# Optimization experiments

Measured on AMD Instinct MI355X. Metric: run time of the kernel, lower is better.

Reference implementation:

```python
import jax, jax.numpy as jnp
import numpy as np

B, T, D_IN, H, K, C = 8, 2048, 512, 384, 8192, 8
N_BLOCKS = 6
EPS = 1e-5


def conv1d(x, w, b, pad, groups=1):
    # x: [B, Cin, T], w: [Cout, Cin//groups, k]
    y = jax.lax.conv_general_dilated(
        x, w, window_strides=(1,), padding=[(pad, pad)],
        dimension_numbers=("NCH", "OIH", "NCH"), feature_group_count=groups)
    return y + b[None, :, None]


def layernorm(x, g, b):
    # normalize over last axis
    m = jnp.mean(x, axis=-1, keepdims=True)
    v = jnp.mean(jnp.square(x - m), axis=-1, keepdims=True)
    return (x - m) * jax.lax.rsqrt(v + EPS) * g + b


def setup_inputs() -> dict:
    key = jax.random.key(0)
    ks = iter(jax.random.split(key, 32))
    s = 0.02
    inp = {
        "x": jax.random.normal(next(ks), (B, T, D_IN), dtype=jnp.float32),
        "enc_w": jax.random.normal(next(ks), (H, D_IN, 7)) * s,
        "enc_b": jnp.zeros((H,)),
        "enc_ln_g": jnp.ones((H,)),
        "enc_ln_b": jnp.zeros((H,)),
        "blk_dw_w": jax.random.normal(next(ks), (N_BLOCKS, H, 1, 7)) * s,
        "blk_dw_b": jnp.zeros((N_BLOCKS, H)),
        "blk_ln_g": jnp.ones((N_BLOCKS, H)),
        "blk_ln_b": jnp.zeros((N_BLOCKS, H)),
        "blk_w1": jax.random.normal(next(ks), (N_BLOCKS, 4 * H, H)) * s,
        "blk_b1": jnp.zeros((N_BLOCKS, 4 * H)),
        "blk_w2": jax.random.normal(next(ks), (N_BLOCKS, H, 4 * H)) * s,
        "blk_b2": jnp.zeros((N_BLOCKS, H)),
        "out_w": jax.random.normal(next(ks), (C, H, 1)) * s,
        "out_b": jnp.zeros((C,)),
        "embeddings": jax.random.normal(next(ks), (K, C)),
    }
    return inp


def encode(x, enc_w, enc_b, enc_ln_g, enc_ln_b, blk_dw_w, blk_dw_b,
           blk_ln_g, blk_ln_b, blk_w1, blk_b1, blk_w2, blk_b2, out_w, out_b):
    h = x.transpose(0, 2, 1)                       # [B, D_IN, T]
    h = conv1d(h, enc_w, enc_b, pad=3)             # [B, H, T]
    h = layernorm(h.transpose(0, 2, 1), enc_ln_g, enc_ln_b).transpose(0, 2, 1)
    for i in range(N_BLOCKS):
        res = h
        h = conv1d(h, blk_dw_w[i], blk_dw_b[i], pad=3, groups=H)  # depthwise
        ht = h.transpose(0, 2, 1)                  # [B, T, H]
        ht = layernorm(ht, blk_ln_g[i], blk_ln_b[i])
        ht = jnp.einsum("bth,fh->btf", ht, blk_w1[i]) + blk_b1[i]
        ht = jax.nn.gelu(ht, approximate=False)    # torch GELU is exact erf
        ht = jnp.einsum("btf,hf->bth", ht, blk_w2[i]) + blk_b2[i]
        h = ht.transpose(0, 2, 1) + res
    z = conv1d(h, out_w, out_b, pad=0)             # [B, C, T]
    return z.transpose(0, 2, 1)                    # [B, T, C]


def reference(x, enc_w, enc_b, enc_ln_g, enc_ln_b, blk_dw_w, blk_dw_b,
              blk_ln_g, blk_ln_b, blk_w1, blk_b1, blk_w2, blk_b2,
              out_w, out_b, embeddings):
    z = encode(x, enc_w, enc_b, enc_ln_g, enc_ln_b, blk_dw_w, blk_dw_b,
               blk_ln_g, blk_ln_b, blk_w1, blk_b1, blk_w2, blk_b2, out_w, out_b)
    flat = z.reshape(-1, C)                        # [B*T, C]
    # squared euclidean distances: same argmin as torch.cdist
    d2 = (jnp.sum(flat * flat, axis=1, keepdims=True)
          - 2.0 * flat @ embeddings.T
          + jnp.sum(embeddings * embeddings, axis=1))  # [B*T, K]
    indices = jnp.argmin(d2, axis=1)               # [B*T], int
    return indices
```

## Files before the change

### kernel.cpp

```cpp
#include <hip/hip_runtime.h>
#include <math.h>

#define T_   2048
#define DIN  512
#define H_   384
#define H4_  1536
#define BT_  16384

typedef _Float16 half_t;
typedef _Float16 f16x8 __attribute__((ext_vector_type(8)));
typedef float f32x4 __attribute__((ext_vector_type(4)));

#define LO_SCALE 2048.0f
#define LO_INV   4.8828125e-4f

__device__ __forceinline__ void lds_barrier() {
    asm volatile("s_waitcnt lgkmcnt(0)\n\ts_barrier" ::: "memory");
}

__device__ __forceinline__ void split2(float v, half_t* hi, half_t* lo) {
    half_t h = (half_t)v;
    *hi = h;
    *lo = (half_t)((v - (float)h) * LO_SCALE);
}

__global__ void k_split(const float* __restrict__ in, half_t* __restrict__ hi,
                        half_t* __restrict__ lo, long n) {
    long i = (long)blockIdx.x * 256 + threadIdx.x;
    if (i >= n) return;
    split2(in[i], hi + i, lo + i);
}

__global__ void k_split_encw(const float* __restrict__ in, half_t* __restrict__ hi,
                             half_t* __restrict__ lo) {
    int idx = blockIdx.x * 256 + threadIdx.x;
    if (idx >= H_ * 3584) return;
    int n = idx / 3584;
    int r = idx % 3584;
    int tap = r >> 9, i = r & 511;
    split2(in[n * 3584 + i * 7 + tap], hi + idx, lo + idx);
}

__global__ void k_ln(const float* __restrict__ in, float* __restrict__ out,
                     const float* __restrict__ g, const float* __restrict__ b) {
    int row = blockIdx.x;
    int lane = threadIdx.x;
    const float* ir = in + (long)row * H_;
    float v[6];
    float s = 0.f;
#pragma unroll
    for (int j = 0; j < 6; ++j) { v[j] = ir[lane + (j << 6)]; s += v[j]; }
#pragma unroll
    for (int o = 32; o > 0; o >>= 1) s += __shfl_down(s, o, 64);
    s = __shfl(s, 0, 64);
    float mean = s * (1.f / 384.f);
    float q = 0.f;
#pragma unroll
    for (int j = 0; j < 6; ++j) { float d = v[j] - mean; q += d * d; }
#pragma unroll
    for (int o = 32; o > 0; o >>= 1) q += __shfl_down(q, o, 64);
    q = __shfl(q, 0, 64);
    float rstd = rsqrtf(q * (1.f / 384.f) + 1e-5f);
    float* orow = out + (long)row * H_;
#pragma unroll
    for (int j = 0; j < 6; ++j) {
        int c = lane + (j << 6);
        orow[c] = (v[j] - mean) * rstd * g[c] + b[c];
    }
}

__global__ __launch_bounds__(256) void k_dwconv_ln(
    const float* __restrict__ h, half_t* __restrict__ oh,
    half_t* __restrict__ ol,
    const float* __restrict__ w, const float* __restrict__ wb,
    const float* __restrict__ g, const float* __restrict__ gb) {
    int row = (blockIdx.x << 2) + (threadIdx.x >> 6);
    int b = row >> 11;
    int t = row & 2047;
    int lane = threadIdx.x & 63;
    const float* hb = h + ((long)b * T_) * H_;
    float vx[3], vy[3];
    float s = 0.f;
#pragma unroll
    for (int j = 0; j < 3; ++j) {
        int c = (lane << 1) + (j << 7);
        float ax = wb[c], ay = wb[c + 1];
        const float* wcx = w + c * 7;
        const float* wcy = wcx + 7;
#pragma unroll
        for (int k = 0; k < 7; ++k) {
            int tt = t + k - 3;
            if ((unsigned)tt < (unsigned)T_) {
                float2 hv = *(const float2*)&hb[(long)tt * H_ + c];
                ax = fmaf(hv.x, wcx[k], ax);
                ay = fmaf(hv.y, wcy[k], ay);
            }
        }
        vx[j] = ax; vy[j] = ay;
        s += ax + ay;
    }
#pragma unroll
    for (int o = 32; o > 0; o >>= 1) s += __shfl_down(s, o, 64);
    s = __shfl(s, 0, 64);
    float mean = s * (1.f / 384.f);
    float q = 0.f;
#pragma unroll
    for (int j = 0; j < 3; ++j) {
        float dx = vx[j] - mean, dy = vy[j] - mean;
        q += dx * dx + dy * dy;
    }
#pragma unroll
    for (int o = 32; o > 0; o >>= 1) q += __shfl_down(q, o, 64);
    q = __shfl(q, 0, 64);
    float rstd = rsqrtf(q * (1.f / 384.f) + 1e-5f);
    long ro = (long)row * H_;
#pragma unroll
    for (int j = 0; j < 3; ++j) {
        int c = (lane << 1) + (j << 7);
        float valx = (vx[j] - mean) * rstd * g[c] + gb[c];
        float valy = (vy[j] - mean) * rstd * g[c + 1] + gb[c + 1];
        split2(valx, oh + ro + c, ol + ro + c);
        split2(valy, oh + ro + c + 1, ol + ro + c + 1);
    }
}

#define DECLSET(S) float4 pAh##S, pAl##S, pBh0##S, pBl0##S, pBh1##S, pBl1##S

#define LOADREGS(S, k0_) do {                                               \
    int k0v = (k0_);                                                        \
    if (MODE == 0) {                                                        \
        int kk = k0v + ak;                                                  \
        int tap = kk >> 9, ii = kk & 511;                                   \
        int ta = tt0 + tap;                                                 \
        pAh##S = pAl##S = make_float4(0.f, 0.f, 0.f, 0.f);                  \
        if ((unsigned)ta < 2048u) {                                         \
            long o = ((long)bq * 2048 + ta) * 512 + ii;                     \
            pAh##S = *(const float4*)(Ah + o);                              \
            pAl##S = *(const float4*)(Al + o);                              \
        }                                                                   \
    } else {                                                                \
        pAh##S = *(const float4*)(Ah + aoff + k0v);                         \
        pAl##S = *(const float4*)(Al + aoff + k0v);                         \
    }                                                                       \
    pBh0##S = *(const float4*)(Bh + boff0 + k0v);                           \
    pBl0##S = *(const float4*)(Bl + boff0 + k0v);                           \
    pBh1##S = *(const float4*)(Bh + boff1 + k0v);                           \
    pBl1##S = *(const float4*)(Bl + boff1 + k0v);                           \
} while (0)

#define STOREBUF(S, buf) do {                                               \
    *(float4*)&smem[(buf) * 2048 + aw] = pAh##S;                            \
    *(float4*)&smem[4096 + (buf) * 2048 + aw] = pAl##S;                     \
    int b_ = 8192 + (buf) * 4096 + aw;                                      \
    *(float4*)&smem[b_] = pBh0##S;                                          \
    *(float4*)&smem[b_ + 2048] = pBh1##S;                                   \
    *(float4*)&smem[b_ + 8192] = pBl0##S;                                   \
    *(float4*)&smem[b_ + 8192 + 2048] = pBl1##S;                            \
} while (0)

template <int MODE, int NN>
__global__ __launch_bounds__(256, 3) void k_mgemm64(
    const half_t* __restrict__ Ah, const half_t* __restrict__ Al,
    const half_t* __restrict__ Bh, const half_t* __restrict__ Bl,
    const float* __restrict__ bias, const float* __restrict__ res,
    float* __restrict__ Cf, half_t* __restrict__ Ch, half_t* __restrict__ Cl,
    int N, int K) {
    __shared__ __align__(16) half_t smem[24576];
    const int tid = threadIdx.x;
    const int lane = tid & 63, wid = tid >> 6;
    const int wn = wid << 5;
    const int quad = lane >> 4, l16 = lane & 15;

    constexpr int NWG = 256 * NN;
    constexpr int CHUNK = NWG / 8;
    const int lin = blockIdx.x;
    const int tile = (lin & 7) * CHUNK + (lin >> 3);
    const int m0 = (tile / NN) << 6;
    const int n0 = (tile % NN) << 7;

    const int ar = tid >> 2;
    const int ak = (tid & 3) << 3;

    long aoff = 0;
    int tt0 = 0, bq = 0;
    if (MODE == 0) {
        bq = m0 >> 11;
        tt0 = (m0 & 2047) + ar - 3;
    } else {
        aoff = (long)(m0 + ar) * K + ak;
    }
    const long boff0 = (long)(n0 + ar) * K + ak;
    const long boff1 = boff0 + (long)64 * K;

    const int aw = ar * 32 + ((((tid & 3) ^ (ar >> 1)) & 3) << 3);

    DECLSET(0);
    DECLSET(1);

    f32x4 acc1[4][2] = {};
    f32x4 acc2[4][2] = {};
    const int sw = ((quad ^ (l16 >> 1)) & 3) << 3;

    auto compute = [&](int buf) {
        const int ab = buf * 2048 + l16 * 32 + sw;
        const int bb = 8192 + buf * 4096 + (wn + l16) * 32 + sw;
        f16x8 fah[4], fal[4], fgh[2], fgl[2];
#pragma unroll
        for (int f = 0; f < 4; ++f) {
            fah[f] = *(const f16x8*)&smem[ab + f * 512];
            fal[f] = *(const f16x8*)&smem[ab + 4096 + f * 512];
        }
#pragma unroll
        for (int g = 0; g < 2; ++g) {
            fgh[g] = *(const f16x8*)&smem[bb + g * 512];
            fgl[g] = *(const f16x8*)&smem[bb + 8192 + g * 512];
        }
#pragma unroll
        for (int f = 0; f < 4; ++f)
#pragma unroll
            for (int g = 0; g < 2; ++g)
                acc2[f][g] = __builtin_amdgcn_mfma_f32_16x16x32_f16(fah[f], fgl[g], acc2[f][g], 0, 0, 0);
#pragma unroll
        for (int f = 0; f < 4; ++f)
#pragma unroll
            for (int g = 0; g < 2; ++g)
                acc2[f][g] = __builtin_amdgcn_mfma_f32_16x16x32_f16(fal[f], fgh[g], acc2[f][g], 0, 0, 0);
#pragma unroll
        for (int f = 0; f < 4; ++f)
#pragma unroll
            for (int g = 0; g < 2; ++g)
                acc1[f][g] = __builtin_amdgcn_mfma_f32_16x16x32_f16(fah[f], fgh[g], acc1[f][g], 0, 0, 0);
    };

    const int nIter = K >> 5;
    LOADREGS(0, 0);
    LOADREGS(1, 32);
    STOREBUF(0, 0);
    if (nIter > 2) LOADREGS(0, 64);
    for (int it = 0; it < nIter; it += 2) {
        lds_barrier();
        compute(0);
        STOREBUF(1, 1);
        if (it + 3 < nIter) LOADREGS(1, (it + 3) << 5);
        lds_barrier();
        compute(1);
        if (it + 2 < nIter) {
            STOREBUF(0, 0);
            if (it + 4 < nIter) LOADREGS(0, (it + 4) << 5);
        }
    }

    float bv[2];
    bv[0] = bias[n0 + wn + l16];
    bv[1] = bias[n0 + wn + 16 + l16];

#pragma unroll
    for (int f = 0; f < 4; ++f)
#pragma unroll
        for (int g = 0; g < 2; ++g)
#pragma unroll
            for (int r = 0; r < 4; ++r) {
                long row = m0 + f * 16 + quad * 4 + r;
                int col = n0 + wn + g * 16 + l16;
                float v = acc1[f][g][r] + acc2[f][g][r] * LO_INV + bv[g];
                long o = row * N + col;
                if (MODE == 2) v += res[o];
                Cf[o] = v;
            }
}

#define LOADW8(k0_) do {                                                    \
    int k0v = (k0_);                                                        \
    qAh = *(const float4*)(Ah + aoff + k0v);                                \
    qAl = *(const float4*)(Al + aoff + k0v);                                \
    if (tid < 384) {                                                        \
        qBh = *(const float4*)(Bh + boff + k0v);                            \
        qBl = *(const float4*)(Bl + boff + k0v);                            \
    }                                                                       \
} while (0)

#define STOREW8(buf) do {                                                   \
    int a_ = (buf) * 14336 + sa;                                            \
    *(float4*)&smem[a_] = qAh;                                              \
    *(float4*)&smem[a_ + 4096] = qAl;                                       \
    if (tid < 384) {                                                        \
        int b_ = (buf) * 14336 + 8192 + sa;                                 \
        *(float4*)&smem[b_] = qBh;                                          \
        *(float4*)&smem[b_ + 3072] = qBl;                                   \
    }                                                                       \
} while (0)

template <int MODE, int NT>
__global__ __launch_bounds__(512, 4) void k_mgemm96w8(
    const half_t* __restrict__ Ah, const half_t* __restrict__ Al,
    const half_t* __restrict__ Bh, const half_t* __restrict__ Bl,
    const float* __restrict__ bias, const float* __restrict__ res,
    float* __restrict__ Cf, half_t* __restrict__ Ch, half_t* __restrict__ Cl,
    int N, int K) {
    __shared__ __align__(16) half_t smem[28672];
    const int tid = threadIdx.x;
    const int lane = tid & 63, wid = tid >> 6;
    const int wm = (wid >> 1) << 5;
    const int wn = (wid & 1) * 48;
    const int quad = lane >> 4, l16 = lane & 15;

    constexpr int NWG = 128 * NT;
    constexpr int CHUNK = NWG / 8;
    const int lin = blockIdx.x;
    const int tile = (lin & 7) * CHUNK + (lin >> 3);
    const int m0 = (tile / NT) << 7;
    const int n0 = (tile % NT) * 96;

    const int srow = tid >> 2;
    const int sg = tid & 3;
    const int sa = srow * 32 + (((sg ^ (tid >> 3)) & 3) << 3);

    const long aoff = (long)(m0 + srow) * K + (sg << 3);
    const long boff = (long)(n0 + srow) * K + (sg << 3);

    float4 qAh, qAl, qBh, qBl;

    f32x4 acc1[2][3] = {};
    f32x4 acc2[2][3] = {};
    const int sw = ((quad ^ (l16 >> 1)) & 3) << 3;

    auto compute = [&](int buf) {
        const int ab = buf * 14336 + (wm + l16) * 32 + sw;
        const int bb = buf * 14336 + 8192 + (wn + l16) * 32 + sw;
        f16x8 fah[2], fal[2], fgh[3], fgl[3];
#pragma unroll
        for (int f = 0; f < 2; ++f) {
            fah[f] = *(const f16x8*)&smem[ab + f * 512];
            fal[f] = *(const f16x8*)&smem[ab + 4096 + f * 512];
        }
#pragma unroll
        for (int g = 0; g < 3; ++g) {
            fgh[g] = *(const f16x8*)&smem[bb + g * 512];
            fgl[g] = *(const f16x8*)&smem[bb + 3072 + g * 512];
        }
#pragma unroll
        for (int f = 0; f < 2; ++f)
#pragma unroll
            for (int g = 0; g < 3; ++g)
                acc2[f][g] = __builtin_amdgcn_mfma_f32_16x16x32_f16(fah[f], fgl[g], acc2[f][g], 0, 0, 0);
#pragma unroll
        for (int f = 0; f < 2; ++f)
#pragma unroll
            for (int g = 0; g < 3; ++g)
                acc2[f][g] = __builtin_amdgcn_mfma_f32_16x16x32_f16(fal[f], fgh[g], acc2[f][g], 0, 0, 0);
#pragma unroll
        for (int f = 0; f < 2; ++f)
#pragma unroll
            for (int g = 0; g < 3; ++g)
                acc1[f][g] = __builtin_amdgcn_mfma_f32_16x16x32_f16(fah[f], fgh[g], acc1[f][g], 0, 0, 0);
    };

    const int nIter = K >> 5;
    LOADW8(0);
    STOREW8(0);
    int cur = 0;
    for (int it = 0; it < nIter; ++it) {
        if (it + 1 < nIter) LOADW8((it + 1) << 5);
        lds_barrier();
        compute(cur);
        if (it + 1 < nIter) STOREW8(cur ^ 1);
        cur ^= 1;
    }

    float bv[3];
#pragma unroll
    for (int g = 0; g < 3; ++g) bv[g] = bias[n0 + wn + g * 16 + l16];

    if (MODE == 1) {
        __syncthreads();
#pragma unroll
        for (int f = 0; f < 2; ++f)
#pragma unroll
            for (int g = 0; g < 3; ++g)
#pragma unroll
                for (int r = 0; r < 4; ++r) {
                    int rm = wm + f * 16 + quad * 4 + r;
                    int cn = wn + g * 16 + l16;
                    float v = acc1[f][g][r] + acc2[f][g][r] * LO_INV + bv[g];
                    v = 0.5f * v * (1.0f + erff(v * 0.70710678118654752f));
                    half_t hh = (half_t)v;
                    smem[rm * 104 + cn] = hh;
                    smem[13312 + rm * 104 + cn] = (half_t)((v - (float)hh) * LO_SCALE);
                }
        __syncthreads();
        int row = tid >> 2, c0 = (tid & 3) * 24;
        long go = (long)(m0 + row) * N + n0 + c0;
        int so = row * 104 + c0;
#pragma unroll
        for (int u = 0; u < 3; ++u) {
            *(float4*)(Ch + go + u * 8) = *(const float4*)&smem[so + u * 8];
            *(float4*)(Cl + go + u * 8) = *(const float4*)&smem[13312 + so + u * 8];
        }
    } else {
#pragma unroll
        for (int f = 0; f < 2; ++f)
#pragma unroll
            for (int g = 0; g < 3; ++g)
#pragma unroll
                for (int r = 0; r < 4; ++r) {
                    long row = m0 + wm + f * 16 + quad * 4 + r;
                    int col = n0 + wn + g * 16 + l16;
                    float v = acc1[f][g][r] + acc2[f][g][r] * LO_INV + bv[g];
                    long o = row * N + col;
                    v += res[o];
                    Cf[o] = v;
                }
    }
}

__global__ __launch_bounds__(256) void k_outconv_argmin(
    const float* __restrict__ h, const float* __restrict__ ow,
    const float* __restrict__ ob, const float* __restrict__ emb,
    int* __restrict__ outIdx) {
    __shared__ float hs[16][H_ + 1];
    __shared__ float zs[16][8];
    __shared__ float es[16 * 516];
    __shared__ float rb[16][16];
    __shared__ int ri[16][16];
    const int tid = threadIdx.x;
    const int row0 = blockIdx.x << 4;

    for (int i = tid; i < 16 * (H_ / 4); i += 256) {
        int r = i / 96;
        int c4 = (i % 96) << 2;
        float4 v = *(const float4*)&h[((long)(row0 + r)) * H_ + c4];
        hs[r][c4] = v.x; hs[r][c4 + 1] = v.y; hs[r][c4 + 2] = v.z; hs[r][c4 + 3] = v.w;
    }
    __syncthreads();

    if (tid < 128) {
        int r = tid & 15, c = tid >> 4;
        float acc = ob[c];
        const float* wc = ow + c * H_;
        for (int j = 0; j < H_; ++j) acc = fmaf(hs[r][j], wc[j], acc);
        zs[r][c] = acc;
    }
    __syncthreads();

    const int r = tid & 15;
    const int sl = tid >> 4;
    float z0 = zs[r][0], z1 = zs[r][1], z2 = zs[r][2], z3 = zs[r][3];
    float z4 = zs[r][4], z5 = zs[r][5], z6 = zs[r][6], z7 = zs[r][7];
    float best = 3.4e38f;
    int bi = 0;

    for (int ch = 0; ch < 8; ++ch) {
        __syncthreads();
        for (int i = tid; i < 2048; i += 256) {
            int e = i >> 1;
            int half = (i & 1) << 2;
            float4 src = *(const float4*)&emb[(((long)(ch << 10)) + e) * 8 + half];
            *(float4*)&es[(e >> 6) * 516 + ((e & 63) << 3) + half] = src;
        }
        __syncthreads();
        const float* ep = es + sl * 516;
        int gbase = (ch << 10) + (sl << 6);
#pragma unroll 4
        for (int j = 0; j < 64; ++j) {
            float4 e0 = *(const float4*)(ep + (j << 3));
            float4 e1 = *(const float4*)(ep + (j << 3) + 4);
            float t, d;
            t = e0.x - z0; d = t * t;
            t = e0.y - z1; d = fmaf(t, t, d);
            t = e0.z - z2; d = fmaf(t, t, d);
            t = e0.w - z3; d = fmaf(t, t, d);
            t = e1.x - z4; d = fmaf(t, t, d);
            t = e1.y - z5; d = fmaf(t, t, d);
            t = e1.z - z6; d = fmaf(t, t, d);
            t = e1.w - z7; d = fmaf(t, t, d);
            if (d < best) { best = d; bi = gbase + j; }
        }
    }
    rb[r][sl] = best;
    ri[r][sl] = bi;
    __syncthreads();
    if (sl == 0) {
        float bb = rb[r][0];
        int bbi = ri[r][0];
#pragma unroll
        for (int s2 = 1; s2 < 16; ++s2) {
            float v = rb[r][s2];
            int i2 = ri[r][s2];
            if (v < bb || (v == bb && i2 < bbi)) { bb = v; bbi = i2; }
        }
        outIdx[row0 + r] = bbi;
    }
}

extern "C" void kernel_launch(void* const* d_in, const int* in_sizes, int n_in,
                              void* d_out, int out_size, void* d_ws, size_t ws_size,
                              hipStream_t stream) {
    const float* x        = (const float*)d_in[0];
    const float* enc_w    = (const float*)d_in[1];
    const float* enc_b    = (const float*)d_in[2];
    const float* enc_ln_g = (const float*)d_in[3];
    const float* enc_ln_b = (const float*)d_in[4];
    const float* blk_dw_w = (const float*)d_in[5];
    const float* blk_dw_b = (const float*)d_in[6];
    const float* blk_ln_g = (const float*)d_in[7];
    const float* blk_ln_b = (const float*)d_in[8];
    const float* blk_w1   = (const float*)d_in[9];
    const float* blk_b1   = (const float*)d_in[10];
    const float* blk_w2   = (const float*)d_in[11];
    const float* blk_b2   = (const float*)d_in[12];
    const float* out_w    = (const float*)d_in[13];
    const float* out_b    = (const float*)d_in[14];
    const float* emb      = (const float*)d_in[15];
    int* out = (int*)d_out;

    char* base = (char*)d_ws;
    float*  h    = (float*)base;
    half_t* tmph = (half_t*)(base + 25165824);
    half_t* tmpl = (half_t*)(base + 37748736);
    half_t* ht4h = (half_t*)(base + 50331648);
    half_t* ht4l = (half_t*)(base + 100663296);
    half_t* ench = (half_t*)(base + 150994944);
    half_t* encl = (half_t*)(base + 153747456);
    half_t* w1h  = (half_t*)(base + 156499968);
    half_t* w1l  = (half_t*)(base + 163577856);
    half_t* w2h  = (half_t*)(base + 170655744);
    half_t* w2l  = (half_t*)(base + 177733632);
    half_t* xh = ht4h;
    half_t* xl = (half_t*)(base + 50331648 + 16777216);

    k_split<<<(8388608 + 255) / 256, 256, 0, stream>>>(x, xh, xl, 8388608L);
    k_split<<<(3538944 + 255) / 256, 256, 0, stream>>>(blk_w1, w1h, w1l, 3538944L);
    k_split<<<(3538944 + 255) / 256, 256, 0, stream>>>(blk_w2, w2h, w2l, 3538944L);
    k_split_encw<<<(H_ * 3584 + 255) / 256, 256, 0, stream>>>(enc_w, ench, encl);

    k_mgemm64<0, 3><<<768, 256, 0, stream>>>(xh, xl, ench, encl, enc_b,
                                             nullptr, h, nullptr, nullptr,
                                             H_, 3584);
    k_ln<<<BT_, 64, 0, stream>>>(h, h, enc_ln_g, enc_ln_b);

    for (int i = 0; i < 6; ++i) {
        k_dwconv_ln<<<BT_ / 4, 256, 0, stream>>>(h, tmph, tmpl, blk_dw_w + i * H_ * 7,
                                                 blk_dw_b + i * H_, blk_ln_g + i * H_,
                                                 blk_ln_b + i * H_);
        k_mgemm96w8<1, 16><<<2048, 512, 0, stream>>>(
            tmph, tmpl, w1h + (long)i * 589824, w1l + (long)i * 589824,
            blk_b1 + i * H4_, nullptr, nullptr, ht4h, ht4l, H4_, H_);
        k_mgemm96w8<2, 4><<<512, 512, 0, stream>>>(
            ht4h, ht4l, w2h + (long)i * 589824, w2l + (long)i * 589824,
            blk_b2 + i * H_, h, h, nullptr, nullptr, H_, H4_);
    }

    k_outconv_argmin<<<BT_ / 16, 256, 0, stream>>>(h, out_w, out_b, emb, out);
}
```

Measured before the change: 1.690 ms.

## Use 128x128 GEMM tiles with direct global-to-LDS DMA loads

Replaces the 128x96, 8-wave block-FFN GEMM with a 128x128, 4-wave kernel where each wave computes a 64x64 sub-tile, raising MFMA work per LDS fragment load. Each wave now stages one of the four operand planes (A hi, A lo, B hi, B lo) with global_load_lds DMA, so data no longer passes through registers into a double-buffered LDS. The GELU/split epilogue is staged through LDS in two half-tile passes to fit the buffer. The trade-offs: the second GEMM launches only 384 blocks, which may underfill the GPU, and the larger accumulator set raises register pressure.

```diff
diff --git a/kernel.cpp b/kernel.cpp
--- a/kernel.cpp
+++ b/kernel.cpp
@@ -16,6 +16,16 @@
 
 __device__ __forceinline__ void lds_barrier() {
     asm volatile("s_waitcnt lgkmcnt(0)\n\ts_barrier" ::: "memory");
+}
+
+__device__ __forceinline__ void vm_barrier() {
+    asm volatile("s_waitcnt vmcnt(0) lgkmcnt(0)\n\ts_barrier" ::: "memory");
+}
+
+__device__ __forceinline__ void gload_lds(const half_t* g, half_t* l) {
+    __builtin_amdgcn_global_load_lds(
+        (const __attribute__((address_space(1))) unsigned int*)(const void*)g,
+        (__attribute__((address_space(3))) unsigned int*)(void*)l, 16, 0, 0);
 }
 
 __device__ __forceinline__ void split2(float v, half_t* hi, half_t* lo) {
@@ -269,39 +279,18 @@
             }
 }
 
-#define LOADW8(k0_) do {                                                    \
-    int k0v = (k0_);                                                        \
-    qAh = *(const float4*)(Ah + aoff + k0v);                                \
-    qAl = *(const float4*)(Al + aoff + k0v);                                \
-    if (tid < 384) {                                                        \
-        qBh = *(const float4*)(Bh + boff + k0v);                            \
-        qBl = *(const float4*)(Bl + boff + k0v);                            \
-    }                                                                       \
-} while (0)
-
-#define STOREW8(buf) do {                                                   \
-    int a_ = (buf) * 14336 + sa;                                            \
-    *(float4*)&smem[a_] = qAh;                                              \
-    *(float4*)&smem[a_ + 4096] = qAl;                                       \
-    if (tid < 384) {                                                        \
-        int b_ = (buf) * 14336 + 8192 + sa;                                 \
-        *(float4*)&smem[b_] = qBh;                                          \
-        *(float4*)&smem[b_ + 3072] = qBl;                                   \
-    }                                                                       \
-} while (0)
-
 template <int MODE, int NT>
-__global__ __launch_bounds__(512, 4) void k_mgemm96w8(
+__global__ __launch_bounds__(256, 2) void k_mgemm128(
     const half_t* __restrict__ Ah, const half_t* __restrict__ Al,
     const half_t* __restrict__ Bh, const half_t* __restrict__ Bl,
     const float* __restrict__ bias, const float* __restrict__ res,
     float* __restrict__ Cf, half_t* __restrict__ Ch, half_t* __restrict__ Cl,
     int N, int K) {
-    __shared__ __align__(16) half_t smem[28672];
+    __shared__ __align__(16) half_t smem[32768];
     const int tid = threadIdx.x;
     const int lane = tid & 63, wid = tid >> 6;
-    const int wm = (wid >> 1) << 5;
-    const int wn = (wid & 1) * 48;
+    const int wm = (wid >> 1) << 6;
+    const int wn = (wid & 1) << 6;
     const int quad = lane >> 4, l16 = lane & 15;
 
     constexpr int NWG = 128 * NT;
@@ -309,98 +298,111 @@
     const int lin = blockIdx.x;
     const int tile = (lin & 7) * CHUNK + (lin >> 3);
     const int m0 = (tile / NT) << 7;
-    const int n0 = (tile % NT) * 96;
-
-    const int srow = tid >> 2;
-    const int sg = tid & 3;
-    const int sa = srow * 32 + (((sg ^ (tid >> 3)) & 3) << 3);
-
-    const long aoff = (long)(m0 + srow) * K + (sg << 3);
-    const long boff = (long)(n0 + srow) * K + (sg << 3);
-
-    float4 qAh, qAl, qBh, qBl;
-
-    f32x4 acc1[2][3] = {};
-    f32x4 acc2[2][3] = {};
+    const int n0 = (tile % NT) << 7;
+
+    const int role = wid;
+    const half_t* srcp = (role == 0) ? Ah : (role == 1) ? Al
+                        : (role == 2) ? Bh : Bl;
+    const int row0g = (role < 2) ? m0 : n0;
+    const int lr = lane >> 2;
+    const int lg = (lane & 3) ^ ((lane >> 3) & 3);
+    const half_t* gbase = srcp + (long)(row0g + lr) * K + lg * 8;
+    const long kstride = (long)16 * K;
+
+#define STAGEDMA(buf, k0_) do {                                             \
+    int k0v = (k0_);                                                        \
+    _Pragma("unroll")                                                       \
+    for (int i_ = 0; i_ < 8; ++i_)                                          \
+        gload_lds(gbase + i_ * kstride + k0v,                               \
+                  &smem[(buf) * 16384 + role * 4096 + i_ * 512]);           \
+} while (0)
+
+    f32x4 acc1[4][4] = {};
+    f32x4 acc2[4][4] = {};
     const int sw = ((quad ^ (l16 >> 1)) & 3) << 3;
 
     auto compute = [&](int buf) {
-        const int ab = buf * 14336 + (wm + l16) * 32 + sw;
-        const int bb = buf * 14336 + 8192 + (wn + l16) * 32 + sw;
-        f16x8 fah[2], fal[2], fgh[3], fgl[3];
-#pragma unroll
-        for (int f = 0; f < 2; ++f) {
+        const int ab = buf * 16384 + (wm + l16) * 32 + sw;
+        const int bb = buf * 16384 + 8192 + (wn + l16) * 32 + sw;
+        f16x8 fah[4], fal[4], fgh[4], fgl[4];
+#pragma unroll
+        for (int f = 0; f < 4; ++f) {
             fah[f] = *(const f16x8*)&smem[ab + f * 512];
             fal[f] = *(const f16x8*)&smem[ab + 4096 + f * 512];
         }
 #pragma unroll
-        for (int g = 0; g < 3; ++g) {
+        for (int g = 0; g < 4; ++g) {
             fgh[g] = *(const f16x8*)&smem[bb + g * 512];
-            fgl[g] = *(const f16x8*)&smem[bb + 3072 + g * 512];
-        }
-#pragma unroll
-        for (int f = 0; f < 2; ++f)
-#pragma unroll
-            for (int g = 0; g < 3; ++g)
+            fgl[g] = *(const f16x8*)&smem[bb + 4096 + g * 512];
+        }
+#pragma unroll
+        for (int f = 0; f < 4; ++f)
+#pragma unroll
+            for (int g = 0; g < 4; ++g)
                 acc2[f][g] = __builtin_amdgcn_mfma_f32_16x16x32_f16(fah[f], fgl[g], acc2[f][g], 0, 0, 0);
 #pragma unroll
-        for (int f = 0; f < 2; ++f)
-#pragma unroll
-            for (int g = 0; g < 3; ++g)
+        for (int f = 0; f < 4; ++f)
+#pragma unroll
+            for (int g = 0; g < 4; ++g)
                 acc2[f][g] = __builtin_amdgcn_mfma_f32_16x16x32_f16(fal[f], fgh[g], acc2[f][g], 0, 0, 0);
 #pragma unroll
-        for (int f = 0; f < 2; ++f)
-#pragma unroll
-            for (int g = 0; g < 3; ++g)
+        for (int f = 0; f < 4; ++f)
+#pragma unroll
+            for (int g = 0; g < 4; ++g)
                 acc1[f][g] = __builtin_amdgcn_mfma_f32_16x16x32_f16(fah[f], fgh[g], acc1[f][g], 0, 0, 0);
     };
 
     const int nIter = K >> 5;
-    LOADW8(0);
-    STOREW8(0);
+    STAGEDMA(0, 0);
+    vm_barrier();
     int cur = 0;
     for (int it = 0; it < nIter; ++it) {
-        if (it + 1 < nIter) LOADW8((it + 1) << 5);
-        lds_barrier();
+        if (it + 1 < nIter) STAGEDMA(cur ^ 1, (it + 1) << 5);
         compute(cur);
-        if (it + 1 < nIter) STOREW8(cur ^ 1);
+        vm_barrier();
         cur ^= 1;
     }
-
-    float bv[3];
-#pragma unroll
-    for (int g = 0; g < 3; ++g) bv[g] = bias[n0 + wn + g * 16 + l16];
+#undef STAGEDMA
+
+    float bv[4];
+#pragma unroll
+    for (int g = 0; g < 4; ++g) bv[g] = bias[n0 + wn + g * 16 + l16];
 
     if (MODE == 1) {
-        __syncthreads();
-#pragma unroll
-        for (int f = 0; f < 2; ++f)
-#pragma unroll
-            for (int g = 0; g < 3; ++g)
-#pragma unroll
-                for (int r = 0; r < 4; ++r) {
-                    int rm = wm + f * 16 + quad * 4 + r;
-                    int cn = wn + g * 16 + l16;
-                    float v = acc1[f][g][r] + acc2[f][g][r] * LO_INV + bv[g];
-                    v = 0.5f * v * (1.0f + erff(v * 0.70710678118654752f));
-                    half_t hh = (half_t)v;
-                    smem[rm * 104 + cn] = hh;
-                    smem[13312 + rm * 104 + cn] = (half_t)((v - (float)hh) * LO_SCALE);
-                }
-        __syncthreads();
-        int row = tid >> 2, c0 = (tid & 3) * 24;
-        long go = (long)(m0 + row) * N + n0 + c0;
-        int so = row * 104 + c0;
-#pragma unroll
-        for (int u = 0; u < 3; ++u) {
-            *(float4*)(Ch + go + u * 8) = *(const float4*)&smem[so + u * 8];
-            *(float4*)(Cl + go + u * 8) = *(const float4*)&smem[13312 + so + u * 8];
+#pragma unroll
+        for (int p = 0; p < 2; ++p) {
+            if ((wid >> 1) == p) {
+#pragma unroll
+                for (int f = 0; f < 4; ++f)
+#pragma unroll
+                    for (int g = 0; g < 4; ++g)
+#pragma unroll
+                        for (int r = 0; r < 4; ++r) {
+                            int rm = f * 16 + quad * 4 + r;
+                            int cn = wn + g * 16 + l16;
+                            float v = acc1[f][g][r] + acc2[f][g][r] * LO_INV + bv[g];
+                            v = 0.5f * v * (1.0f + erff(v * 0.70710678118654752f));
+                            half_t hh = (half_t)v;
+                            smem[rm * 136 + cn] = hh;
+                            smem[8704 + rm * 136 + cn] = (half_t)((v - (float)hh) * LO_SCALE);
+                        }
+            }
+            __syncthreads();
+            int rrow = tid >> 2, c0 = (tid & 3) << 5;
+            long go = (long)(m0 + p * 64 + rrow) * N + n0 + c0;
+            int so = rrow * 136 + c0;
+#pragma unroll
+            for (int u = 0; u < 4; ++u) {
+                *(float4*)(Ch + go + u * 8) = *(const float4*)&smem[so + u * 8];
+                *(float4*)(Cl + go + u * 8) = *(const float4*)&smem[8704 + so + u * 8];
+            }
+            __syncthreads();
         }
     } else {
 #pragma unroll
-        for (int f = 0; f < 2; ++f)
-#pragma unroll
-            for (int g = 0; g < 3; ++g)
+        for (int f = 0; f < 4; ++f)
+#pragma unroll
+            for (int g = 0; g < 4; ++g)
 #pragma unroll
                 for (int r = 0; r < 4; ++r) {
                     long row = m0 + wm + f * 16 + quad * 4 + r;
@@ -542,10 +544,10 @@
         k_dwconv_ln<<<BT_ / 4, 256, 0, stream>>>(h, tmph, tmpl, blk_dw_w + i * H_ * 7,
                                                  blk_dw_b + i * H_, blk_ln_g + i * H_,
                                                  blk_ln_b + i * H_);
-        k_mgemm96w8<1, 16><<<2048, 512, 0, stream>>>(
+        k_mgemm128<1, 12><<<1536, 256, 0, stream>>>(
             tmph, tmpl, w1h + (long)i * 589824, w1l + (long)i * 589824,
             blk_b1 + i * H4_, nullptr, nullptr, ht4h, ht4l, H4_, H_);
-        k_mgemm96w8<2, 4><<<512, 512, 0, stream>>>(
+        k_mgemm128<2, 3><<<384, 256, 0, stream>>>(
             ht4h, ht4l, w2h + (long)i * 589824, w2l + (long)i * 589824,
             blk_b2 + i * H_, h, h, nullptr, nullptr, H_, H4_);
     }
```

Result: slower. 1.752 ms (+3.7%).
